# Optimization experiments

Hardware: AMD Instinct MI355X
Metric: run time of the kernel (lower is better)

Reference implementation:

```python
import jax, jax.numpy as jnp
import numpy as np

N = 50000      # nodes
E = 800000     # edges (avg degree 16)
INDIM = 128
OUTDIM = 64


def setup_inputs() -> dict:
    key = jax.random.key(0)
    k1, k2, k3, k4, k5 = jax.random.split(key, 5)
    h = jax.random.normal(k1, (N, INDIM), dtype=jnp.float32)
    W = jax.random.normal(k2, (INDIM, OUTDIM), dtype=jnp.float32) * 0.05
    Wa = jax.random.normal(k3, (2 * OUTDIM,), dtype=jnp.float32) * 0.05
    src = jax.random.randint(k4, (E,), 0, N)
    dst = jax.random.randint(k5, (E,), 0, N)
    return {"h": h, "W": W, "Wa": Wa, "src": src, "dst": dst}


def reference(h, W, Wa, src, dst):
    # node transform: n_mlp_layer=1, bias=False MultiLinearLayer == one linear
    z = h @ W  # [N, OUTDIM]
    # edge attention: relu(attn_linear(cat(z_src, z_dst)))
    # avoid materializing [E, 2*OUTDIM] concat: split Wa into src/dst halves
    s = z @ Wa[:OUTDIM]   # [N] src contribution
    t = z @ Wa[OUTDIM:]   # [N] dst contribution
    e = jax.nn.relu(s[src] + t[dst])  # [E]
    # segment softmax over incoming edges of each destination node
    m = jax.ops.segment_max(e, dst, num_segments=N)      # [N]
    ex = jnp.exp(e - m[dst])                             # [E]
    denom = jax.ops.segment_sum(ex, dst, num_segments=N) # [N]
    alpha = ex / denom[dst]                              # [E]
    # weighted scatter-sum aggregation of src features (dropout p=0 -> identity)
    h_out = jax.ops.segment_sum(alpha[:, None] * z[src], dst, num_segments=N)
    # batch_norm=False; final activation relu; dropout p=0 -> identity
    return jax.nn.relu(h_out)
```

## Files before the change

kernel.cpp:

```cpp
#include <hip/hip_runtime.h>
#include <math.h>

#define INDIM 128
#define OUTDIM 64
#define HK 136
#define CP 68
#define SCHUNK 2048

typedef __bf16 bf16x8 __attribute__((ext_vector_type(8)));
typedef float f32x4 __attribute__((ext_vector_type(4)));
typedef unsigned short ushortx8 __attribute__((ext_vector_type(8)));

static __device__ __forceinline__ unsigned short f2bf(float f) {
    unsigned u = __float_as_uint(f);
    u += 0x7FFFu + ((u >> 16) & 1u);
    return (unsigned short)(u >> 16);
}
static __device__ __forceinline__ float bf2f(unsigned short b) {
    return __uint_as_float((unsigned)b << 16);
}

__global__ __launch_bounds__(256) void nt_count(
    const float* __restrict__ h, const float* __restrict__ W,
    const float* __restrict__ Wa, unsigned short* __restrict__ z,
    float* __restrict__ s, float* __restrict__ t,
    const int* __restrict__ dst, int* __restrict__ bcnt,
    int N, int E, int gemm_blocks)
{
    __shared__ __align__(16) unsigned short smem[2 * 64 * HK];
    unsigned short* As = smem;
    unsigned short* Bs = smem + 64 * HK;
    float* Cs = (float*)smem;
    int tid = threadIdx.x;

    if (blockIdx.x >= gemm_blocks) {
        int* l = (int*)smem;
        l[tid] = 0;
        __syncthreads();
        int base = (blockIdx.x - gemm_blocks) * 8192;
        #pragma unroll 4
        for (int u = 0; u < 32; ++u) {
            int i = base + u * 256 + tid;
            if (i < E) atomicAdd(&l[dst[i] >> 8], 1);
        }
        __syncthreads();
        if (l[tid]) atomicAdd(bcnt + tid, l[tid]);
        return;
    }

    int node0 = blockIdx.x * 64;
    int nv = min(64, N - node0);

    {
        const float4* hg = (const float4*)(h + (size_t)node0 * INDIM);
        #pragma unroll
        for (int i = 0; i < 8; ++i) {
            int idx = i * 256 + tid;
            int n = idx >> 5, j = idx & 31;
            float4 v = (n < nv) ? hg[n * 32 + j] : make_float4(0.f, 0.f, 0.f, 0.f);
            ushort4 b = make_ushort4(f2bf(v.x), f2bf(v.y), f2bf(v.z), f2bf(v.w));
            *(ushort4*)&As[n * HK + j * 4] = b;
        }
    }
    {
        int n = tid & 63, kg = tid >> 6;
        const float* Wc = W + n;
        #pragma unroll
        for (int uu = 0; uu < 8; ++uu) {
            int k = kg * 32 + uu * 4;
            ushort4 b = make_ushort4(f2bf(Wc[(k + 0) * OUTDIM]),
                                     f2bf(Wc[(k + 1) * OUTDIM]),
                                     f2bf(Wc[(k + 2) * OUTDIM]),
                                     f2bf(Wc[(k + 3) * OUTDIM]));
            *(ushort4*)&Bs[n * HK + k] = b;
        }
    }
    __syncthreads();

    int wv = tid >> 6, l = tid & 63;
    int lr = l & 15, lg = l >> 4;

    f32x4 acc[4];
    #pragma unroll
    for (int nf = 0; nf < 4; ++nf) acc[nf] = (f32x4){0.f, 0.f, 0.f, 0.f};

    #pragma unroll
    for (int ks = 0; ks < 4; ++ks) {
        int k0 = ks * 32 + lg * 8;
        bf16x8 a = *(const bf16x8*)&As[(wv * 16 + lr) * HK + k0];
        #pragma unroll
        for (int nf = 0; nf < 4; ++nf) {
            bf16x8 b = *(const bf16x8*)&Bs[(nf * 16 + lr) * HK + k0];
            acc[nf] = __builtin_amdgcn_mfma_f32_16x16x32_bf16(a, b, acc[nf], 0, 0, 0);
        }
    }

    __syncthreads();

    #pragma unroll
    for (int nf = 0; nf < 4; ++nf)
        #pragma unroll
        for (int r = 0; r < 4; ++r)
            Cs[(wv * 16 + lg * 4 + r) * CP + nf * 16 + lr] = acc[nf][r];

    int row = wv * 16 + (l >> 2);
    int cq = l & 3;
    int node = node0 + row;
    float ssum = 0.f, tsum = 0.f;
    #pragma unroll
    for (int qq = 0; qq < 2; ++qq) {
        int c0 = cq * 16 + qq * 8;
        float4 ca = *(const float4*)&Cs[row * CP + c0];
        float4 cb = *(const float4*)&Cs[row * CP + c0 + 4];
        float4 wsa = *(const float4*)&Wa[c0];
        float4 wsb = *(const float4*)&Wa[c0 + 4];
        float4 wta = *(const float4*)&Wa[OUTDIM + c0];
        float4 wtb = *(const float4*)&Wa[OUTDIM + c0 + 4];
        ssum += ca.x * wsa.x + ca.y * wsa.y + ca.z * wsa.z + ca.w * wsa.w
              + cb.x * wsb.x + cb.y * wsb.y + cb.z * wsb.z + cb.w * wsb.w;
        tsum += ca.x * wta.x + ca.y * wta.y + ca.z * wta.z + ca.w * wta.w
              + cb.x * wtb.x + cb.y * wtb.y + cb.z * wtb.z + cb.w * wtb.w;
        if (node < N) {
            ushortx8 zb;
            zb[0] = f2bf(ca.x); zb[1] = f2bf(ca.y);
            zb[2] = f2bf(ca.z); zb[3] = f2bf(ca.w);
            zb[4] = f2bf(cb.x); zb[5] = f2bf(cb.y);
            zb[6] = f2bf(cb.z); zb[7] = f2bf(cb.w);
            *(ushortx8*)&z[(size_t)node * OUTDIM + c0] = zb;
        }
    }
    ssum += __shfl_xor(ssum, 1, 64);
    ssum += __shfl_xor(ssum, 2, 64);
    tsum += __shfl_xor(tsum, 1, 64);
    tsum += __shfl_xor(tsum, 2, 64);
    if (cq == 0 && node < N) {
        s[node] = ssum;
        t[node] = tsum;
    }
}

__global__ __launch_bounds__(256) void bucket_scatter(
    const int* __restrict__ src, const int* __restrict__ dst,
    const int* __restrict__ bcnt, int* __restrict__ gcursor,
    int* __restrict__ esort, int E)
{
    __shared__ int lcnt[256];
    __shared__ int loff[256];
    __shared__ int gbase[256];
    __shared__ int lcur[256];
    __shared__ int bs[256];
    __shared__ int stage[SCHUNK];
    __shared__ unsigned char bof[SCHUNK];
    int tid = threadIdx.x;
    int base = blockIdx.x * SCHUNK;
    int ne = min(SCHUNK, E - base);

    int bc = bcnt[tid];
    bs[tid] = bc;
    lcnt[tid] = 0;
    __syncthreads();
    for (int off = 1; off < 256; off <<= 1) {
        int add = (tid >= off) ? bs[tid - off] : 0;
        __syncthreads();
        bs[tid] += add;
        __syncthreads();
    }
    int bstart_own = bs[tid] - bc;

    int mys[8], myd[8];
    #pragma unroll
    for (int u = 0; u < 8; ++u) {
        int li = u * 256 + tid;
        if (li < ne) {
            mys[u] = src[base + li];
            myd[u] = dst[base + li];
            atomicAdd(&lcnt[myd[u] >> 8], 1);
        } else myd[u] = -1;
    }
    __syncthreads();

    loff[tid] = lcnt[tid];
    __syncthreads();
    for (int off = 1; off < 256; off <<= 1) {
        int add = (tid >= off) ? loff[tid - off] : 0;
        __syncthreads();
        loff[tid] += add;
        __syncthreads();
    }
    int excl = loff[tid] - lcnt[tid];
    loff[tid] = excl;
    lcur[tid] = excl;
    if (lcnt[tid] > 0)
        gbase[tid] = bstart_own + atomicAdd(gcursor + tid, lcnt[tid]);
    __syncthreads();

    #pragma unroll
    for (int u = 0; u < 8; ++u) {
        if (myd[u] >= 0) {
            int b = myd[u] >> 8;
            int p = atomicAdd(&lcur[b], 1);
            stage[p] = ((myd[u] & 255) << 24) | mys[u];
            bof[p] = (unsigned char)b;
        }
    }
    __syncthreads();

    for (int i = tid; i < ne; i += 256) {
        int b = bof[i];
        esort[gbase[b] + (i - loff[b])] = stage[i];
    }
}

__global__ __launch_bounds__(256) void bucket_fill(
    const int* __restrict__ esort, const int* __restrict__ bcnt,
    int* __restrict__ counts, int* __restrict__ offsets,
    int* __restrict__ srcs, int N)
{
    __shared__ int bs[256];
    __shared__ int cnt[256];
    __shared__ int off[256];
    __shared__ int cur[256];
    int tid = threadIdx.x;
    int b = blockIdx.x;

    int bc = bcnt[tid];
    bs[tid] = bc;
    cnt[tid] = 0;
    __syncthreads();
    for (int o = 1; o < 256; o <<= 1) {
        int add = (tid >= o) ? bs[tid - o] : 0;
        __syncthreads();
        bs[tid] += add;
        __syncthreads();
    }
    int e0 = (b > 0) ? bs[b - 1] : 0;
    int e1 = bs[b];
    int node0 = b << 8;

    for (int i = e0 + tid; i < e1; i += 256)
        atomicAdd(&cnt[((unsigned)esort[i]) >> 24], 1);
    __syncthreads();

    off[tid] = cnt[tid];
    __syncthreads();
    for (int o = 1; o < 256; o <<= 1) {
        int add = (tid >= o) ? off[tid - o] : 0;
        __syncthreads();
        off[tid] += add;
        __syncthreads();
    }
    int excl = off[tid] - cnt[tid];
    cur[tid] = excl;
    int node = node0 + tid;
    if (node < N) { counts[node] = cnt[tid]; offsets[node] = e0 + excl; }
    __syncthreads();

    for (int i = e0 + tid; i < e1; i += 256) {
        int pe = esort[i];
        int p = atomicAdd(&cur[((unsigned)pe) >> 24], 1);
        srcs[e0 + p] = pe & 0xFFFFFF;
    }
}

__global__ __launch_bounds__(256) void aggregate(
    const unsigned short* __restrict__ z, const int* __restrict__ srcs,
    const float* __restrict__ s, const float* __restrict__ t,
    const int* __restrict__ offsets, const int* __restrict__ counts,
    float* __restrict__ out, int N)
{
    __shared__ int   ls[8][64];
    __shared__ float le[8][64];
    int hw = threadIdx.x >> 5;
    int lane = threadIdx.x & 31;
    int node = blockIdx.x * 8 + hw;
    if (node >= N) return;
    int start = offsets[node];
    int deg = counts[node];
    float2 acc = make_float2(0.f, 0.f);

    if (deg > 0) {
        float tn = t[node];
        float se = 0.f;
        for (int c0 = 0; c0 < deg; c0 += 64) {
            int cn = min(64, deg - c0);
            float pe = 0.f;
            if (lane < cn) {
                int sj = srcs[start + c0 + lane];
                float e = __expf(fmaxf(s[sj] + tn, 0.f));
                ls[hw][lane] = sj; le[hw][lane] = e; pe += e;
            }
            if (lane + 32 < cn) {
                int sj = srcs[start + c0 + lane + 32];
                float e = __expf(fmaxf(s[sj] + tn, 0.f));
                ls[hw][lane + 32] = sj; le[hw][lane + 32] = e; pe += e;
            }
            #pragma unroll
            for (int off = 16; off; off >>= 1) pe += __shfl_xor(pe, off, 32);
            se += pe;

            int j = 0;
            for (; j + 8 <= cn; j += 8) {
                int si[8]; float ei[8]; ushort2 ai[8];
                #pragma unroll
                for (int u = 0; u < 8; ++u) { si[u] = ls[hw][j + u]; ei[u] = le[hw][j + u]; }
                #pragma unroll
                for (int u = 0; u < 8; ++u)
                    ai[u] = *(const ushort2*)&z[(size_t)si[u] * OUTDIM + lane * 2];
                #pragma unroll
                for (int u = 0; u < 8; ++u) {
                    acc.x += ei[u] * bf2f(ai[u].x);
                    acc.y += ei[u] * bf2f(ai[u].y);
                }
            }
            for (; j < cn; ++j) {
                int sj = ls[hw][j]; float ej = le[hw][j];
                ushort2 a = *(const ushort2*)&z[(size_t)sj * OUTDIM + lane * 2];
                acc.x += ej * bf2f(a.x);
                acc.y += ej * bf2f(a.y);
            }
        }
        float inv = 1.f / se;
        acc.x = fmaxf(acc.x * inv, 0.f);
        acc.y = fmaxf(acc.y * inv, 0.f);
    }
    *(float2*)&out[(size_t)node * OUTDIM + lane * 2] = acc;
}

extern "C" void kernel_launch(void* const* d_in, const int* in_sizes, int n_in,
                              void* d_out, int out_size, void* d_ws, size_t ws_size,
                              hipStream_t stream) {
    const float* h  = (const float*)d_in[0];
    const float* W  = (const float*)d_in[1];
    const float* Wa = (const float*)d_in[2];
    const int* src  = (const int*)d_in[3];
    const int* dst  = (const int*)d_in[4];
    int N = in_sizes[0] / INDIM;
    int E = in_sizes[3];
    float* out = (float*)d_out;
    int nbuck = (N + 255) >> 8;

    char* ws = (char*)d_ws;
    unsigned short* z = (unsigned short*)ws;  ws += (size_t)N * OUTDIM * 2;
    float* s       = (float*)ws;  ws += (size_t)N * 4;
    float* t       = (float*)ws;  ws += (size_t)N * 4;
    int*   srcs    = (int*)ws;    ws += (size_t)E * 4;
    int*   counts  = (int*)ws;    ws += (size_t)N * 4;
    int*   offsets = (int*)ws;    ws += (size_t)N * 4;
    int*   esort   = (int*)ws;    ws += (size_t)E * 4;
    int*   bcnt    = (int*)ws;    ws += 256 * 4;
    int*   gcursor = (int*)ws;    ws += 256 * 4;

    int gemm_blocks = (N + 63) / 64;
    int count_blocks = (E + 8191) / 8192;

    hipMemsetAsync(bcnt, 0, 512 * sizeof(int), stream);

    nt_count<<<gemm_blocks + count_blocks, 256, 0, stream>>>(
        h, W, Wa, z, s, t, dst, bcnt, N, E, gemm_blocks);
    bucket_scatter<<<(E + SCHUNK - 1) / SCHUNK, 256, 0, stream>>>(
        src, dst, bcnt, gcursor, esort, E);
    bucket_fill<<<nbuck, 256, 0, stream>>>(esort, bcnt, counts, offsets, srcs, N);
    aggregate<<<(N + 7) / 8, 256, 0, stream>>>(z, srcs, s, t, offsets, counts, out, N);
}
```

Baseline: 141.6 us.

## Replace two-pass bucket sort with per-node counting and atomic cursor scatter

The two-level bucket sort of edges by destination (bucket_scatter into an intermediate esort array, then bucket_fill) is replaced by per-node degree counting in the count phase via global atomics. A scan kernel then turns bucket totals and per-node counts into offsets and cursors, and a simple edge_scatter places each src with an atomicAdd on its destination's cursor. This removes the esort intermediate and the staging and local scans, in exchange for about 800K global atomics per pass, contended across nodes. The order of edges within a segment becomes nondeterministic.

```diff
diff --git a/kernel.cpp b/kernel.cpp
--- a/kernel.cpp
+++ b/kernel.cpp
@@ -5,7 +5,6 @@
 #define OUTDIM 64
 #define HK 136
 #define CP 68
-#define SCHUNK 2048
 
 typedef __bf16 bf16x8 __attribute__((ext_vector_type(8)));
 typedef float f32x4 __attribute__((ext_vector_type(4)));
@@ -25,6 +24,7 @@
     const float* __restrict__ Wa, unsigned short* __restrict__ z,
     float* __restrict__ s, float* __restrict__ t,
     const int* __restrict__ dst, int* __restrict__ bcnt,
+    int* __restrict__ counts,
     int N, int E, int gemm_blocks)
 {
     __shared__ __align__(16) unsigned short smem[2 * 64 * HK];
@@ -41,7 +41,11 @@
         #pragma unroll 4
         for (int u = 0; u < 32; ++u) {
             int i = base + u * 256 + tid;
-            if (i < E) atomicAdd(&l[dst[i] >> 8], 1);
+            if (i < E) {
+                int d = dst[i];
+                atomicAdd(&l[d >> 8], 1);
+                atomicAdd(&counts[d], 1);
+            }
         }
         __syncthreads();
         if (l[tid]) atomicAdd(bcnt + tid, l[tid]);
@@ -139,126 +143,46 @@
     }
 }
 
-__global__ __launch_bounds__(256) void bucket_scatter(
-    const int* __restrict__ src, const int* __restrict__ dst,
-    const int* __restrict__ bcnt, int* __restrict__ gcursor,
-    int* __restrict__ esort, int E)
-{
-    __shared__ int lcnt[256];
-    __shared__ int loff[256];
-    __shared__ int gbase[256];
-    __shared__ int lcur[256];
+__global__ __launch_bounds__(256) void scan_offsets(
+    const int* __restrict__ counts, const int* __restrict__ bcnt,
+    int* __restrict__ offsets, int* __restrict__ cursor)
+{
     __shared__ int bs[256];
-    __shared__ int stage[SCHUNK];
-    __shared__ unsigned char bof[SCHUNK];
-    int tid = threadIdx.x;
-    int base = blockIdx.x * SCHUNK;
-    int ne = min(SCHUNK, E - base);
-
-    int bc = bcnt[tid];
-    bs[tid] = bc;
-    lcnt[tid] = 0;
-    __syncthreads();
-    for (int off = 1; off < 256; off <<= 1) {
-        int add = (tid >= off) ? bs[tid - off] : 0;
-        __syncthreads();
-        bs[tid] += add;
-        __syncthreads();
-    }
-    int bstart_own = bs[tid] - bc;
-
-    int mys[8], myd[8];
-    #pragma unroll
-    for (int u = 0; u < 8; ++u) {
-        int li = u * 256 + tid;
-        if (li < ne) {
-            mys[u] = src[base + li];
-            myd[u] = dst[base + li];
-            atomicAdd(&lcnt[myd[u] >> 8], 1);
-        } else myd[u] = -1;
-    }
-    __syncthreads();
-
-    loff[tid] = lcnt[tid];
-    __syncthreads();
-    for (int off = 1; off < 256; off <<= 1) {
-        int add = (tid >= off) ? loff[tid - off] : 0;
-        __syncthreads();
-        loff[tid] += add;
-        __syncthreads();
-    }
-    int excl = loff[tid] - lcnt[tid];
-    loff[tid] = excl;
-    lcur[tid] = excl;
-    if (lcnt[tid] > 0)
-        gbase[tid] = bstart_own + atomicAdd(gcursor + tid, lcnt[tid]);
-    __syncthreads();
-
-    #pragma unroll
-    for (int u = 0; u < 8; ++u) {
-        if (myd[u] >= 0) {
-            int b = myd[u] >> 8;
-            int p = atomicAdd(&lcur[b], 1);
-            stage[p] = ((myd[u] & 255) << 24) | mys[u];
-            bof[p] = (unsigned char)b;
-        }
-    }
-    __syncthreads();
-
-    for (int i = tid; i < ne; i += 256) {
-        int b = bof[i];
-        esort[gbase[b] + (i - loff[b])] = stage[i];
-    }
-}
-
-__global__ __launch_bounds__(256) void bucket_fill(
-    const int* __restrict__ esort, const int* __restrict__ bcnt,
-    int* __restrict__ counts, int* __restrict__ offsets,
-    int* __restrict__ srcs, int N)
-{
-    __shared__ int bs[256];
-    __shared__ int cnt[256];
-    __shared__ int off[256];
-    __shared__ int cur[256];
+    __shared__ int cs[256];
     int tid = threadIdx.x;
     int b = blockIdx.x;
 
-    int bc = bcnt[tid];
-    bs[tid] = bc;
-    cnt[tid] = 0;
+    bs[tid] = bcnt[tid];
+    int n = b * 256 + tid;
+    int c = counts[n];
+    cs[tid] = c;
     __syncthreads();
     for (int o = 1; o < 256; o <<= 1) {
-        int add = (tid >= o) ? bs[tid - o] : 0;
-        __syncthreads();
-        bs[tid] += add;
-        __syncthreads();
-    }
-    int e0 = (b > 0) ? bs[b - 1] : 0;
-    int e1 = bs[b];
-    int node0 = b << 8;
-
-    for (int i = e0 + tid; i < e1; i += 256)
-        atomicAdd(&cnt[((unsigned)esort[i]) >> 24], 1);
-    __syncthreads();
-
-    off[tid] = cnt[tid];
-    __syncthreads();
-    for (int o = 1; o < 256; o <<= 1) {
-        int add = (tid >= o) ? off[tid - o] : 0;
-        __syncthreads();
-        off[tid] += add;
-        __syncthreads();
-    }
-    int excl = off[tid] - cnt[tid];
-    cur[tid] = excl;
-    int node = node0 + tid;
-    if (node < N) { counts[node] = cnt[tid]; offsets[node] = e0 + excl; }
-    __syncthreads();
-
-    for (int i = e0 + tid; i < e1; i += 256) {
-        int pe = esort[i];
-        int p = atomicAdd(&cur[((unsigned)pe) >> 24], 1);
-        srcs[e0 + p] = pe & 0xFFFFFF;
+        int addb = (tid >= o) ? bs[tid - o] : 0;
+        int addc = (tid >= o) ? cs[tid - o] : 0;
+        __syncthreads();
+        bs[tid] += addb;
+        cs[tid] += addc;
+        __syncthreads();
+    }
+    int base = (b > 0) ? bs[b - 1] : 0;
+    int off = base + cs[tid] - c;
+    offsets[n] = off;
+    cursor[n] = off;
+}
+
+__global__ __launch_bounds__(256) void edge_scatter(
+    const int* __restrict__ src, const int* __restrict__ dst,
+    int* __restrict__ cursor, int* __restrict__ srcs, int E)
+{
+    int i = blockIdx.x * 2048 + threadIdx.x;
+    #pragma unroll 8
+    for (int u = 0; u < 8; ++u, i += 256) {
+        if (i < E) {
+            int d = dst[i];
+            int p = atomicAdd(&cursor[d], 1);
+            srcs[p] = src[i];
+        }
     }
 }
 
@@ -338,27 +262,26 @@
     int E = in_sizes[3];
     float* out = (float*)d_out;
     int nbuck = (N + 255) >> 8;
+    int NR = nbuck << 8;
 
     char* ws = (char*)d_ws;
     unsigned short* z = (unsigned short*)ws;  ws += (size_t)N * OUTDIM * 2;
     float* s       = (float*)ws;  ws += (size_t)N * 4;
     float* t       = (float*)ws;  ws += (size_t)N * 4;
     int*   srcs    = (int*)ws;    ws += (size_t)E * 4;
-    int*   counts  = (int*)ws;    ws += (size_t)N * 4;
-    int*   offsets = (int*)ws;    ws += (size_t)N * 4;
-    int*   esort   = (int*)ws;    ws += (size_t)E * 4;
+    int*   counts  = (int*)ws;    ws += (size_t)NR * 4;
     int*   bcnt    = (int*)ws;    ws += 256 * 4;
-    int*   gcursor = (int*)ws;    ws += 256 * 4;
+    int*   offsets = (int*)ws;    ws += (size_t)NR * 4;
+    int*   cursor  = (int*)ws;    ws += (size_t)NR * 4;
 
     int gemm_blocks = (N + 63) / 64;
     int count_blocks = (E + 8191) / 8192;
 
-    hipMemsetAsync(bcnt, 0, 512 * sizeof(int), stream);
+    hipMemsetAsync(counts, 0, ((size_t)NR + 256) * sizeof(int), stream);
 
     nt_count<<<gemm_blocks + count_blocks, 256, 0, stream>>>(
-        h, W, Wa, z, s, t, dst, bcnt, N, E, gemm_blocks);
-    bucket_scatter<<<(E + SCHUNK - 1) / SCHUNK, 256, 0, stream>>>(
-        src, dst, bcnt, gcursor, esort, E);
-    bucket_fill<<<nbuck, 256, 0, stream>>>(esort, bcnt, counts, offsets, srcs, N);
+        h, W, Wa, z, s, t, dst, bcnt, counts, N, E, gemm_blocks);
+    scan_offsets<<<nbuck, 256, 0, stream>>>(counts, bcnt, offsets, cursor);
+    edge_scatter<<<(E + 2047) / 2048, 256, 0, stream>>>(src, dst, cursor, srcs, E);
     aggregate<<<(N + 7) / 8, 256, 0, stream>>>(z, srcs, s, t, offsets, counts, out, N);
 }
```

Result: slower. 198.7 us (+40.3%).
